# Optimization experiments

Measured on AMD Instinct MI355X. Metric: run time of the kernel, lower is better.

Reference implementation:

```python
import jax, jax.numpy as jnp
import numpy as np

B, D_IN, H, T = 8192, 5000, 512, 16

def setup_inputs() -> dict:
    key = jax.random.key(0)
    ks = jax.random.split(key, 7)
    s_mlp = 1.0 / np.sqrt(D_IN)
    s_cla = 1.0 / np.sqrt(H)
    return {
        "data_input": jax.random.normal(ks[0], (B, D_IN), jnp.float32),
        "mlp_w": jax.random.normal(ks[1], (H, D_IN), jnp.float32) * s_mlp,
        "mlp_b": jax.random.normal(ks[2], (H,), jnp.float32) * s_mlp,
        "CM": jax.random.normal(ks[3], (T, H, H), jnp.float32) * (1.0 / np.sqrt(H)),
        "attn": jax.random.normal(ks[4], (H, T), jnp.float32) * (1.0 / np.sqrt(H)),
        "cla_w": jax.random.normal(ks[5], (1, H), jnp.float32) * s_cla,
        "cla_b": jax.random.normal(ks[6], (1,), jnp.float32) * s_cla,
    }

def reference(data_input, mlp_w, mlp_b, CM, attn, cla_w, cla_b):
    # mlp_out: [B,H]  (dropout p=0 -> identity)
    mlp_out = data_input @ mlp_w.T + mlp_b
    # task attention weights: softmax over tasks, [B,T]
    w = jax.nn.softmax(mlp_out @ attn, axis=1)
    # Fused mixture-of-matrices apply: out[b,k] = sum_t w[b,t] * sum_h mlp_out[b,h] * CM[t,h,k]
    # Avoids materializing the [B,T,H,H] tensor of the original.
    btk = jnp.einsum('bh,thk->btk', mlp_out, CM)   # [B,T,H]
    mlp_out_1 = jnp.einsum('bt,btk->bk', w, btk)   # [B,H]
    # classifier + sigmoid, squeeze -> [B]
    logits = mlp_out_1 @ cla_w.T + cla_b           # [B,1]
    return jax.nn.sigmoid(logits)[:, 0]
```

## Files before the change

### kernel.cpp

```cpp
#include <hip/hip_runtime.h>
#include <hip/hip_bf16.h>
#include <stdint.h>

typedef __bf16 bf16x8 __attribute__((ext_vector_type(8)));
typedef float f32x4 __attribute__((ext_vector_type(4)));


__device__ __forceinline__ void gld_lds16(const void* g, void* l) {
  __builtin_amdgcn_global_load_lds(
      (const __attribute__((address_space(1))) unsigned int*)g,
      (__attribute__((address_space(3))) unsigned int*)l, 16, 0, 0);
}

__device__ __forceinline__ uint16_t f2bf(float f) {
  uint32_t u = __float_as_uint(f);
  return (uint16_t)((u + 0x7fffu + ((u >> 16) & 1u)) >> 16);
}

__device__ __forceinline__ uint32_t pk2(float a, float b) {
  return (uint32_t)f2bf(a) | ((uint32_t)f2bf(b) << 16);
}

union BF8U {
  uint32_t u[4];
  bf16x8 v;
};

__device__ __forceinline__ bf16x8 pack8(float4 f0, float4 f1) {
  BF8U r;
  r.u[0] = pk2(f0.x, f0.y);
  r.u[1] = pk2(f0.z, f0.w);
  r.u[2] = pk2(f1.x, f1.y);
  r.u[3] = pk2(f1.z, f1.w);
  return r.v;
}

__global__ __launch_bounds__(256) void cmv_kernel(const float* __restrict__ CM,
                                                  const float* __restrict__ cla_w,
                                                  float* __restrict__ Vs) {
  const int tid = threadIdx.x, lane = tid & 63, wid = tid >> 6;
  const int row = blockIdx.x * 4 + wid;
  const float4* src = (const float4*)(CM + (int64_t)row * 512);
  const float4* cw = (const float4*)cla_w;
  float4 a0 = src[lane * 2], a1 = src[lane * 2 + 1];
  float4 w0 = cw[lane * 2], w1 = cw[lane * 2 + 1];
  float s = a0.x * w0.x + a0.y * w0.y + a0.z * w0.z + a0.w * w0.w +
            a1.x * w1.x + a1.y * w1.y + a1.z * w1.z + a1.w * w1.w;
#pragma unroll
  for (int o = 32; o >= 1; o >>= 1) s += __shfl_xor(s, o);
  if (lane == 0) {
    int t = row >> 9, h = row & 511;
    Vs[h * 16 + t] = s;
  }
}

__global__ __launch_bounds__(256) void gmake(const float* __restrict__ mlp_w,
                                             const float* __restrict__ attn,
                                             const float* __restrict__ Vs,
                                             float* __restrict__ Gp) {
  __shared__ float Us[128 * 32];
  const int tid = threadIdx.x;
  const int k = blockIdx.x * 256 + tid;
  const int z = blockIdx.y;
  const int h0 = z * 128;
#pragma unroll
  for (int p = 0; p < 4; ++p) {
    int e4 = p * 256 + tid;
    int h = e4 >> 3, c4 = e4 & 7;
    float4 v;
    if (c4 < 4)
      v = ((const float4*)(attn + (h0 + h) * 16))[c4];
    else
      v = ((const float4*)(Vs + (h0 + h) * 16))[c4 - 4];
    *(float4*)&Us[h * 32 + c4 * 4] = v;
  }
  __syncthreads();
  float acc[32];
#pragma unroll
  for (int c = 0; c < 32; ++c) acc[c] = 0.f;
  const bool valid = (k < 5000);
  const float* wp = mlp_w + (int64_t)h0 * 5000 + (valid ? k : 0);
  for (int h = 0; h < 128; ++h) {
    float a = valid ? wp[(int64_t)h * 5000] : 0.f;
    const float4* ur = (const float4*)&Us[h * 32];
#pragma unroll
    for (int c4 = 0; c4 < 8; ++c4) {
      float4 u = ur[c4];
      acc[c4 * 4 + 0] += a * u.x;
      acc[c4 * 4 + 1] += a * u.y;
      acc[c4 * 4 + 2] += a * u.z;
      acc[c4 * 4 + 3] += a * u.w;
    }
  }
  float* gp = Gp + (int64_t)z * 32 * 5120 + k;
#pragma unroll
  for (int c = 0; c < 32; ++c) gp[(int64_t)c * 5120] = acc[c];
}

__global__ void gfinal(const float* __restrict__ Gp,
                       uint16_t* __restrict__ Gt) {
  int e8 = blockIdx.x * 256 + threadIdx.x;
  const float4* p = (const float4*)(Gp) + (int64_t)e8 * 2;
  const int64_t pl = 32 * 5120 / 4;
  float4 a0 = p[0], a1 = p[1];
#pragma unroll
  for (int z = 1; z < 4; ++z) {
    float4 b0 = p[z * pl], b1 = p[z * pl + 1];
    a0.x += b0.x; a0.y += b0.y; a0.z += b0.z; a0.w += b0.w;
    a1.x += b1.x; a1.y += b1.y; a1.z += b1.z; a1.w += b1.w;
  }
  uint4 v = make_uint4(pk2(a0.x, a0.y), pk2(a0.z, a0.w),
                       pk2(a1.x, a1.y), pk2(a1.z, a1.w));
  ((uint4*)Gt)[e8] = v;
}

__global__ __launch_bounds__(256) void cbias(const float* __restrict__ mlp_b,
                                             const float* __restrict__ attn,
                                             const float* __restrict__ Vs,
                                             float* __restrict__ cvec) {
  __shared__ float red[256];
  const int tid = threadIdx.x;
  const int c = tid & 31, g = tid >> 5;
  float acc = 0.f;
  for (int h = g; h < 512; h += 8) {
    float bv = mlp_b[h];
    float uv = (c < 16) ? attn[h * 16 + c] : Vs[h * 16 + (c - 16)];
    acc += bv * uv;
  }
  red[tid] = acc;
  __syncthreads();
  if (tid < 32) {
    float s = 0.f;
#pragma unroll
    for (int g2 = 0; g2 < 8; ++g2) s += red[g2 * 32 + tid];
    cvec[tid] = s;
  }
}

__global__ __launch_bounds__(256, 4) void megagemm(
    const float* __restrict__ A,
    const uint16_t* __restrict__ Gt,
    float* __restrict__ P) {
  __shared__ __align__(16) uint16_t Gs[32 * 640];
  const int tid = threadIdx.x;
  const int lane = tid & 63;
  const int w = tid >> 6;
  const int lin = blockIdx.x;
  const int mb = lin & 127;
  const int z = lin >> 7;
  const int m0 = mb * 64;
  const int k0 = z * 640;

#pragma unroll
  for (int p = 0; p < 10; ++p) {
    int e = p * 256 + tid;
    int row = e / 80;
    int c8 = e - row * 80;
    int src8 = (c8 & 0x78) | ((c8 ^ row) & 7);
    gld_lds16(Gt + (int64_t)row * 5120 + k0 + src8 * 8, &Gs[e * 8]);
  }
  __syncthreads();

  const int lr = lane & 15;
  const int kg = lane >> 4;
  const int key = lr & 7;
  const float* Arow = A + (int64_t)(m0 + w * 16 + lr) * 5000;

  f32x4 acc0 = {}, acc1 = {};
#pragma unroll
  for (int step = 0; step < 20; ++step) {
    const int col = k0 + step * 32 + kg * 8;
    const float4* s = (const float4*)(Arow + (col < 5000 ? col : 0));
    float4 f0 = s[0], f1 = s[1];
    bf16x8 af = pack8(f0, f1);
    const int ch = (step * 4 + kg) ^ key;
    bf16x8 b0 = *(const bf16x8*)&Gs[lr * 640 + ch * 8];
    bf16x8 b1 = *(const bf16x8*)&Gs[(16 + lr) * 640 + ch * 8];
    acc0 = __builtin_amdgcn_mfma_f32_16x16x32_bf16(af, b0, acc0, 0, 0, 0);
    acc1 = __builtin_amdgcn_mfma_f32_16x16x32_bf16(af, b1, acc1, 0, 0, 0);
  }

  float* Pz = P + ((int64_t)z * 8192 + m0 + w * 16) * 32;
#pragma unroll
  for (int r = 0; r < 4; ++r) {
    int row = kg * 4 + r;
    Pz[row * 32 + lr] = acc0[r];
    Pz[row * 32 + 16 + lr] = acc1[r];
  }
}

__global__ __launch_bounds__(256) void epilogue(
    const float* __restrict__ P, const float* __restrict__ cvec,
    const float* __restrict__ cla_b, float* __restrict__ out) {
  const int tid = threadIdx.x;
  const int row = blockIdx.x * 8 + (tid >> 5);
  const int c = tid & 31;
  float s = cvec[c];
#pragma unroll
  for (int z = 0; z < 8; ++z)
    s += P[((int64_t)z * 8192 + row) * 32 + c];
  float yv = __shfl_xor(s, 16);
  float m = s;
#pragma unroll
  for (int o = 8; o >= 1; o >>= 1) m = fmaxf(m, __shfl_xor(m, o));
  float e = __expf(s - m);
  float sum = e;
#pragma unroll
  for (int o = 8; o >= 1; o >>= 1) sum += __shfl_xor(sum, o);
  float val = (e / sum) * yv;
#pragma unroll
  for (int o = 8; o >= 1; o >>= 1) val += __shfl_xor(val, o);
  if (c == 0) out[row] = 1.f / (1.f + __expf(-(val + cla_b[0])));
}

extern "C" void kernel_launch(void* const* d_in, const int* in_sizes, int n_in,
                              void* d_out, int out_size, void* d_ws,
                              size_t ws_size, hipStream_t stream) {
  const float* data = (const float*)d_in[0];
  const float* mlp_w = (const float*)d_in[1];
  const float* mlp_b = (const float*)d_in[2];
  const float* CM = (const float*)d_in[3];
  const float* attn = (const float*)d_in[4];
  const float* cla_w = (const float*)d_in[5];
  const float* cla_b = (const float*)d_in[6];
  float* out = (float*)d_out;

  char* ws = (char*)d_ws;
  uint16_t* Gt = (uint16_t*)(ws + 0);
  float* Gp = (float*)(ws + 327680);
  float* Vs = (float*)(ws + 2949120);
  float* cvec = (float*)(ws + 2981888);
  float* P = (float*)(ws + 2982016);

  cmv_kernel<<<2048, 256, 0, stream>>>(CM, cla_w, Vs);
  gmake<<<dim3(20, 4), 256, 0, stream>>>(mlp_w, attn, Vs, Gp);
  gfinal<<<80, 256, 0, stream>>>(Gp, Gt);
  cbias<<<1, 256, 0, stream>>>(mlp_b, attn, Vs, cvec);
  megagemm<<<1024, 256, 0, stream>>>(data, Gt, P);
  epilogue<<<1024, 256, 0, stream>>>(P, cvec, cla_b, out);
}
```

Before: 322.0 us.

## Fuse G construction, partial reduction and bias into one kernel

Replaces the gmake, gfinal and cbias kernels with one kernel, gmake3. Each block splits the h range across its four waves and sums the four partials in shared memory before writing bf16 G directly, and one extra block computes the bias vector. This drops two launches and the fp32 partial-sum round trip through global memory, at the cost of uncoalesced 2-byte stores and per-h reads of attn/Vs from global memory. Separately, megagemm drops the column bounds check for the K-slices that are fully in range.

```diff
diff --git a/kernel.cpp b/kernel.cpp
--- a/kernel.cpp
+++ b/kernel.cpp
@@ -54,86 +54,75 @@
   }
 }
 
-__global__ __launch_bounds__(256) void gmake(const float* __restrict__ mlp_w,
-                                             const float* __restrict__ attn,
-                                             const float* __restrict__ Vs,
-                                             float* __restrict__ Gp) {
-  __shared__ float Us[128 * 32];
+__global__ __launch_bounds__(256) void gmake3(
+    const float* __restrict__ mlp_w, const float* __restrict__ mlp_b,
+    const float* __restrict__ attn, const float* __restrict__ Vs,
+    uint16_t* __restrict__ Gt, float* __restrict__ cvec) {
   const int tid = threadIdx.x;
-  const int k = blockIdx.x * 256 + tid;
-  const int z = blockIdx.y;
-  const int h0 = z * 128;
-#pragma unroll
-  for (int p = 0; p < 4; ++p) {
-    int e4 = p * 256 + tid;
-    int h = e4 >> 3, c4 = e4 & 7;
-    float4 v;
-    if (c4 < 4)
-      v = ((const float4*)(attn + (h0 + h) * 16))[c4];
-    else
-      v = ((const float4*)(Vs + (h0 + h) * 16))[c4 - 4];
-    *(float4*)&Us[h * 32 + c4 * 4] = v;
-  }
+  if (blockIdx.x == 80) {
+    __shared__ float red[256];
+    const int c = tid & 31, g = tid >> 5;
+    float acc = 0.f;
+    for (int h = g; h < 512; h += 8) {
+      float uv = (c < 16) ? attn[h * 16 + c] : Vs[h * 16 + (c - 16)];
+      acc += mlp_b[h] * uv;
+    }
+    red[tid] = acc;
+    __syncthreads();
+    if (tid < 32) {
+      float s = 0.f;
+#pragma unroll
+      for (int g2 = 0; g2 < 8; ++g2) s += red[g2 * 32 + tid];
+      cvec[tid] = s;
+    }
+    return;
+  }
+
+  __shared__ float Ls[4 * 64 * 33];
+  const int kl = tid & 63;
+  const int wv = tid >> 6;
+  const int k = blockIdx.x * 64 + kl;
+  const bool valid = (k < 5000);
+  const float* wp = mlp_w + (valid ? k : 0);
+  const int h0 = wv * 128;
+
+  float acc[32];
+#pragma unroll
+  for (int c = 0; c < 32; ++c) acc[c] = 0.f;
+
+  for (int hh = 0; hh < 128; ++hh) {
+    const int h = h0 + hh;
+    float a = valid ? wp[(int64_t)h * 5000] : 0.f;
+    const float4* ar = (const float4*)(attn + h * 16);
+    const float4* vr = (const float4*)(Vs + h * 16);
+#pragma unroll
+    for (int q = 0; q < 4; ++q) {
+      float4 u = ar[q];
+      acc[q * 4 + 0] += a * u.x;
+      acc[q * 4 + 1] += a * u.y;
+      acc[q * 4 + 2] += a * u.z;
+      acc[q * 4 + 3] += a * u.w;
+    }
+#pragma unroll
+    for (int q = 0; q < 4; ++q) {
+      float4 u = vr[q];
+      acc[16 + q * 4 + 0] += a * u.x;
+      acc[16 + q * 4 + 1] += a * u.y;
+      acc[16 + q * 4 + 2] += a * u.z;
+      acc[16 + q * 4 + 3] += a * u.w;
+    }
+  }
+  float* lp = Ls + (wv * 64 + kl) * 33;
+#pragma unroll
+  for (int c = 0; c < 32; ++c) lp[c] = acc[c];
   __syncthreads();
-  float acc[32];
-#pragma unroll
-  for (int c = 0; c < 32; ++c) acc[c] = 0.f;
-  const bool valid = (k < 5000);
-  const float* wp = mlp_w + (int64_t)h0 * 5000 + (valid ? k : 0);
-  for (int h = 0; h < 128; ++h) {
-    float a = valid ? wp[(int64_t)h * 5000] : 0.f;
-    const float4* ur = (const float4*)&Us[h * 32];
-#pragma unroll
-    for (int c4 = 0; c4 < 8; ++c4) {
-      float4 u = ur[c4];
-      acc[c4 * 4 + 0] += a * u.x;
-      acc[c4 * 4 + 1] += a * u.y;
-      acc[c4 * 4 + 2] += a * u.z;
-      acc[c4 * 4 + 3] += a * u.w;
-    }
-  }
-  float* gp = Gp + (int64_t)z * 32 * 5120 + k;
-#pragma unroll
-  for (int c = 0; c < 32; ++c) gp[(int64_t)c * 5120] = acc[c];
-}
-
-__global__ void gfinal(const float* __restrict__ Gp,
-                       uint16_t* __restrict__ Gt) {
-  int e8 = blockIdx.x * 256 + threadIdx.x;
-  const float4* p = (const float4*)(Gp) + (int64_t)e8 * 2;
-  const int64_t pl = 32 * 5120 / 4;
-  float4 a0 = p[0], a1 = p[1];
-#pragma unroll
-  for (int z = 1; z < 4; ++z) {
-    float4 b0 = p[z * pl], b1 = p[z * pl + 1];
-    a0.x += b0.x; a0.y += b0.y; a0.z += b0.z; a0.w += b0.w;
-    a1.x += b1.x; a1.y += b1.y; a1.z += b1.z; a1.w += b1.w;
-  }
-  uint4 v = make_uint4(pk2(a0.x, a0.y), pk2(a0.z, a0.w),
-                       pk2(a1.x, a1.y), pk2(a1.z, a1.w));
-  ((uint4*)Gt)[e8] = v;
-}
-
-__global__ __launch_bounds__(256) void cbias(const float* __restrict__ mlp_b,
-                                             const float* __restrict__ attn,
-                                             const float* __restrict__ Vs,
-                                             float* __restrict__ cvec) {
-  __shared__ float red[256];
-  const int tid = threadIdx.x;
-  const int c = tid & 31, g = tid >> 5;
-  float acc = 0.f;
-  for (int h = g; h < 512; h += 8) {
-    float bv = mlp_b[h];
-    float uv = (c < 16) ? attn[h * 16 + c] : Vs[h * 16 + (c - 16)];
-    acc += bv * uv;
-  }
-  red[tid] = acc;
-  __syncthreads();
-  if (tid < 32) {
-    float s = 0.f;
-#pragma unroll
-    for (int g2 = 0; g2 < 8; ++g2) s += red[g2 * 32 + tid];
-    cvec[tid] = s;
+#pragma unroll
+  for (int p = 0; p < 8; ++p) {
+    int e = p * 256 + tid;
+    int kk = e >> 5, c = e & 31;
+    float s = Ls[kk * 33 + c] + Ls[(64 + kk) * 33 + c] +
+              Ls[(128 + kk) * 33 + c] + Ls[(192 + kk) * 33 + c];
+    Gt[(int64_t)c * 5120 + blockIdx.x * 64 + kk] = f2bf(s);
   }
 }
 
@@ -167,17 +156,32 @@
   const float* Arow = A + (int64_t)(m0 + w * 16 + lr) * 5000;
 
   f32x4 acc0 = {}, acc1 = {};
-#pragma unroll
-  for (int step = 0; step < 20; ++step) {
-    const int col = k0 + step * 32 + kg * 8;
-    const float4* s = (const float4*)(Arow + (col < 5000 ? col : 0));
-    float4 f0 = s[0], f1 = s[1];
-    bf16x8 af = pack8(f0, f1);
-    const int ch = (step * 4 + kg) ^ key;
-    bf16x8 b0 = *(const bf16x8*)&Gs[lr * 640 + ch * 8];
-    bf16x8 b1 = *(const bf16x8*)&Gs[(16 + lr) * 640 + ch * 8];
-    acc0 = __builtin_amdgcn_mfma_f32_16x16x32_bf16(af, b0, acc0, 0, 0, 0);
-    acc1 = __builtin_amdgcn_mfma_f32_16x16x32_bf16(af, b1, acc1, 0, 0, 0);
+  if (z < 7) {
+#pragma unroll
+    for (int step = 0; step < 20; ++step) {
+      const int col = k0 + step * 32 + kg * 8;
+      const float4* s = (const float4*)(Arow + col);
+      float4 f0 = s[0], f1 = s[1];
+      bf16x8 af = pack8(f0, f1);
+      const int ch = (step * 4 + kg) ^ key;
+      bf16x8 b0 = *(const bf16x8*)&Gs[lr * 640 + ch * 8];
+      bf16x8 b1 = *(const bf16x8*)&Gs[(16 + lr) * 640 + ch * 8];
+      acc0 = __builtin_amdgcn_mfma_f32_16x16x32_bf16(af, b0, acc0, 0, 0, 0);
+      acc1 = __builtin_amdgcn_mfma_f32_16x16x32_bf16(af, b1, acc1, 0, 0, 0);
+    }
+  } else {
+#pragma unroll
+    for (int step = 0; step < 20; ++step) {
+      const int col = k0 + step * 32 + kg * 8;
+      const float4* s = (const float4*)(Arow + (col < 5000 ? col : 0));
+      float4 f0 = s[0], f1 = s[1];
+      bf16x8 af = pack8(f0, f1);
+      const int ch = (step * 4 + kg) ^ key;
+      bf16x8 b0 = *(const bf16x8*)&Gs[lr * 640 + ch * 8];
+      bf16x8 b1 = *(const bf16x8*)&Gs[(16 + lr) * 640 + ch * 8];
+      acc0 = __builtin_amdgcn_mfma_f32_16x16x32_bf16(af, b0, acc0, 0, 0, 0);
+      acc1 = __builtin_amdgcn_mfma_f32_16x16x32_bf16(af, b1, acc1, 0, 0, 0);
+    }
   }
 
   float* Pz = P + ((int64_t)z * 8192 + m0 + w * 16) * 32;
@@ -227,15 +231,12 @@
 
   char* ws = (char*)d_ws;
   uint16_t* Gt = (uint16_t*)(ws + 0);
-  float* Gp = (float*)(ws + 327680);
-  float* Vs = (float*)(ws + 2949120);
-  float* cvec = (float*)(ws + 2981888);
-  float* P = (float*)(ws + 2982016);
+  float* Vs = (float*)(ws + 327680);
+  float* cvec = (float*)(ws + 360448);
+  float* P = (float*)(ws + 360576);
 
   cmv_kernel<<<2048, 256, 0, stream>>>(CM, cla_w, Vs);
-  gmake<<<dim3(20, 4), 256, 0, stream>>>(mlp_w, attn, Vs, Gp);
-  gfinal<<<80, 256, 0, stream>>>(Gp, Gt);
-  cbias<<<1, 256, 0, stream>>>(mlp_b, attn, Vs, cvec);
+  gmake3<<<81, 256, 0, stream>>>(mlp_w, mlp_b, attn, Vs, Gt, cvec);
   megagemm<<<1024, 256, 0, stream>>>(data, Gt, P);
   epilogue<<<1024, 256, 0, stream>>>(P, cvec, cla_b, out);
 }
```

Result: faster. 310.6 us (-3.5%).
